# Kernel optimization log

Hardware: AMD Instinct MI355X
Metric: run time of the kernel (lower is better)

The kernel has to match this reference:

```python
import jax, jax.numpy as jnp
import numpy as np
from jax import lax

B, D, T = 16, 256, 8192
N_CB, CB_SIZE, CB_DIM = 7, 1024, 8
EPS = 1e-12


def setup_inputs() -> dict:
    key = jax.random.key(0)
    ks = jax.random.split(key, 9)
    z = jax.random.normal(ks[0], (B, D, T), dtype=jnp.float32)
    # weight-normalized 1x1 conv params (v direction, g magnitude, bias)
    in_v = jax.random.normal(ks[1], (N_CB, CB_DIM, D), dtype=jnp.float32) * 0.05
    in_g = jax.random.uniform(ks[2], (N_CB, CB_DIM), minval=0.5, maxval=1.5, dtype=jnp.float32)
    in_b = jax.random.normal(ks[3], (N_CB, CB_DIM), dtype=jnp.float32) * 0.01
    out_v = jax.random.normal(ks[4], (N_CB, D, CB_DIM), dtype=jnp.float32) * 0.05
    out_g = jax.random.uniform(ks[5], (N_CB, D), minval=0.5, maxval=1.5, dtype=jnp.float32)
    out_b = jax.random.normal(ks[6], (N_CB, D), dtype=jnp.float32) * 0.01
    codebooks = jax.random.normal(ks[7], (N_CB, CB_SIZE, CB_DIM), dtype=jnp.float32)
    return {"z": z, "in_v": in_v, "in_g": in_g, "in_b": in_b,
            "out_v": out_v, "out_g": out_g, "out_b": out_b,
            "codebooks": codebooks, "n_quantizers": 7}


def _wn(v, g):
    # torch weight_norm dim=0: per-output-channel direction * magnitude
    return g[:, None] * v / jnp.linalg.norm(v, axis=1, keepdims=True)


def _l2norm(x):
    return x / jnp.maximum(jnp.linalg.norm(x, axis=-1, keepdims=True), EPS)


def reference(z, in_v, in_g, in_b, out_v, out_g, out_b, codebooks, n_quantizers):
    b = z.shape[0]
    residual = z
    z_q = jnp.zeros_like(z)
    commitment_loss = jnp.float32(0.0)
    codebook_loss = jnp.float32(0.0)
    all_indices = []
    for i in range(N_CB):
        w_in = _wn(in_v[i], in_g[i])            # [cd, D]
        z_e = jnp.einsum('cd,bdt->bct', w_in, residual) + in_b[i][None, :, None]  # [B, cd, T]
        enc = z_e.transpose(0, 2, 1).reshape(-1, CB_DIM)        # [(B T), cd]
        enc_n = _l2norm(enc)
        cb_n = _l2norm(codebooks[i])                             # [K, cd]
        dist = (jnp.sum(enc_n**2, axis=1, keepdims=True)
                - 2.0 * enc_n @ cb_n.T
                + jnp.sum(cb_n**2, axis=1)[None, :])             # [(B T), K]
        idx = jnp.argmin(dist, axis=1).reshape(b, -1)            # [B, T]
        z_q_c = codebooks[i][idx].transpose(0, 2, 1)             # [B, cd, T]
        commit_i = jnp.mean((z_e - lax.stop_gradient(z_q_c))**2, axis=(1, 2))  # [B]
        cbl_i = jnp.mean((z_q_c - lax.stop_gradient(z_e))**2, axis=(1, 2))     # [B]
        z_q_ste = z_e + lax.stop_gradient(z_q_c - z_e)
        w_out = _wn(out_v[i], out_g[i])          # [D, cd]
        z_q_i = jnp.einsum('dc,bct->bdt', w_out, z_q_ste) + out_b[i][None, :, None]
        mask = (jnp.full((b,), i) < n_quantizers).astype(z.dtype)  # [B]
        z_q = z_q + z_q_i * mask[:, None, None]
        residual = residual - z_q_i
        commitment_loss = commitment_loss + jnp.mean(commit_i * mask)
        codebook_loss = codebook_loss + jnp.mean(cbl_i * mask)
        all_indices.append(idx)
    return z_q, commitment_loss, codebook_loss, jnp.stack(all_indices, axis=1)
```

## Files before the change

kernel.cpp:

```cpp
#include <hip/hip_runtime.h>
#include <math.h>

#define NCB 7
#define CBK 1024
#define CD  8
#define BB  16
#define DD  256
#define TT  8192

static constexpr size_t ZQN  = (size_t)BB * DD * TT;
static constexpr size_t IDX0 = ZQN + 2;

__global__ void rvq_prep(const float* __restrict__ in_v, const float* __restrict__ in_g,
                         const float* __restrict__ out_v, const float* __restrict__ out_g,
                         const float* __restrict__ cb,
                         float* __restrict__ wTin, float* __restrict__ wTout,
                         float* __restrict__ cbp, double* __restrict__ lossAcc)
{
#pragma clang fp contract(off)
  int gid = blockIdx.x * blockDim.x + threadIdx.x;
  if (gid == 0) *lossAcc = 0.0;
  if (gid < NCB*DD*CD) {
    int i = gid / (DD*CD); int rem = gid % (DD*CD); int d = rem / CD; int c = rem % CD;
    const float* vrow = in_v + ((size_t)i*CD + c) * DD;
    double acc = 0.0;
    for (int q = 0; q < DD; ++q) { double v = vrow[q]; acc += v*v; }
    float nf = (float)sqrt(acc);
    wTin[((size_t)i*DD + d)*CD + c] = (in_g[i*CD + c] * vrow[d]) / nf;
  } else if (gid < 2*NCB*DD*CD) {
    int e = gid - NCB*DD*CD;
    int i = e / (DD*CD); int rem = e % (DD*CD); int d = rem / CD; int c = rem % CD;
    const float* vrow = out_v + ((size_t)i*DD + d)*CD;
    double acc = 0.0;
    for (int q = 0; q < CD; ++q) { double v = vrow[q]; acc += v*v; }
    float nf = (float)sqrt(acc);
    wTout[((size_t)i*DD + d)*CD + c] = (out_g[i*DD + d] * vrow[c]) / nf;
  } else if (gid < 2*NCB*DD*CD + NCB*CBK) {
    int e = gid - 2*NCB*DD*CD;
    int i = e / CBK; int k = e % CBK;
    const float* row = cb + ((size_t)i*CBK + k)*CD;
    double acc = 0.0;
    for (int c = 0; c < CD; ++c) { double v = row[c]; acc += v*v; }
    float nf = fmaxf((float)sqrt(acc), 1e-12f);
    float* orow = cbp + ((size_t)i*CBK + k)*16;
    float c2 = 0.f;
    for (int c = 0; c < CD; ++c) {
      float cn = row[c] / nf;
      orow[c] = cn;
      float q = cn*cn; c2 += q;
    }
    orow[8] = c2;
  }
}

__launch_bounds__(256, 2)
__global__ void rvq_main(const float* __restrict__ z,
                         const float* __restrict__ in_b, const float* __restrict__ out_b,
                         const float* __restrict__ cb,
                         const int* __restrict__ nqp,
                         const float* __restrict__ wTin, const float* __restrict__ wTout,
                         const float* __restrict__ cbp,
                         float* __restrict__ out, double* __restrict__ lossAcc)
{
#pragma clang fp contract(off)
  const int tid = threadIdx.x;
  const int p   = tid & 63;
  const int wu  = __builtin_amdgcn_readfirstlane(tid >> 6);
  const int blk = blockIdx.x;
  const int b   = blk >> 7;
  const int t0  = (blk & 127) << 6;
  int nq = *nqp; nq = nq < 0 ? 0 : (nq > NCB ? NCB : nq);

  __shared__ float zep[4][64][CD];
  __shared__ float encn[64][CD];
  __shared__ float zef[64][CD];
  __shared__ float aval[64];
  __shared__ float bdist[4][64];
  __shared__ int   bkix[4][64];
  __shared__ float zst[64][CD];

  const float* zbase = z + ((size_t)b*DD + wu*64)*TT + t0 + p;
  float* zqbase = out + ((size_t)b*DD + wu*64)*TT + t0 + p;

  float r[64];
#pragma unroll
  for (int j = 0; j < 64; ++j) r[j] = zbase[(size_t)j*TT];

  if (nq == 0) {
#pragma unroll 8
    for (int j = 0; j < 64; ++j) zqbase[(size_t)j*TT] = 0.f;
  }

  double lacc = 0.0;

  for (int i = 0; i < NCB; ++i) {
    float ze[CD];
#pragma unroll
    for (int c = 0; c < CD; ++c) ze[c] = 0.f;
    const float* wrow = wTin + ((size_t)i*DD + wu*64)*CD;
#pragma unroll 8
    for (int j = 0; j < 64; ++j) {
      float rv = r[j];
#pragma unroll
      for (int c = 0; c < CD; ++c) ze[c] = fmaf(wrow[j*CD + c], rv, ze[c]);
    }
#pragma unroll
    for (int c = 0; c < CD; ++c) zep[wu][p][c] = ze[c];
    __syncthreads();

    if (tid < 64) {
      float zfull[CD];
#pragma unroll
      for (int c = 0; c < CD; ++c) {
        float s = ((zep[0][p][c] + zep[1][p][c]) + zep[2][p][c]) + zep[3][p][c];
        zfull[c] = s + in_b[i*CD + c];
      }
      float ss = 0.f;
#pragma unroll
      for (int c = 0; c < CD; ++c) { float q = zfull[c]*zfull[c]; ss += q; }
      float den = fmaxf(sqrtf(ss), 1e-12f);
      float a2 = 0.f;
#pragma unroll
      for (int c = 0; c < CD; ++c) {
        float en = zfull[c] / den;
        encn[p][c] = en;
        zef[p][c]  = zfull[c];
        float q = en*en; a2 += q;
      }
      aval[p] = a2;
    }
    __syncthreads();

    float en[CD];
#pragma unroll
    for (int c = 0; c < CD; ++c) en[c] = encn[p][c];
    float a2 = aval[p];
    const float* crow = cbp + ((size_t)i*CBK + wu*256)*16;
    float best = 3.0e38f; int bk = 0;
#pragma unroll 4
    for (int kk = 0; kk < 256; ++kk) {
      const float* rw = crow + kk*16;
      float m = en[0]*rw[0];
#pragma unroll
      for (int c = 1; c < CD; ++c) m = fmaf(en[c], rw[c], m);
      float dd = fmaf(-2.f, m, a2) + rw[8];
      bool lt = dd < best;
      best = lt ? dd : best;
      bk   = lt ? kk : bk;
    }
    bdist[wu][p] = best; bkix[wu][p] = wu*256 + bk;
    __syncthreads();

    if (tid < 64) {
      float bb_ = bdist[0][p]; int k = bkix[0][p];
#pragma unroll
      for (int ww = 1; ww < 4; ++ww) {
        float dv = bdist[ww][p]; int kv = bkix[ww][p];
        bool lt = dv < bb_;
        bb_ = lt ? dv : bb_;
        k   = lt ? kv : k;
      }
      const float* qrow = cb + ((size_t)i*CBK + k)*CD;
      float sloc = 0.f;
#pragma unroll
      for (int c = 0; c < CD; ++c) {
        float zc = qrow[c];
        float zv = zef[p][c];
        zst[p][c] = zv + (zc - zv);
        float df = zv - zc;
        float q = df*df; sloc += q;
      }
      if (i < nq) lacc += (double)sloc;
      out[IDX0 + ((size_t)b*NCB + i)*TT + t0 + p] = (float)k;
    }
    __syncthreads();

    float zs[CD];
#pragma unroll
    for (int c = 0; c < CD; ++c) zs[c] = zst[p][c];
    const float* worow = wTout + ((size_t)i*DD + wu*64)*CD;
    const float* obrow = out_b + i*DD + wu*64;
#pragma unroll 8
    for (int j = 0; j < 64; ++j) {
      float m = worow[j*CD]*zs[0];
#pragma unroll
      for (int c = 1; c < CD; ++c) m = fmaf(worow[j*CD + c], zs[c], m);
      float zqi = m + obrow[j];
      r[j] -= zqi;
    }
    if (i == nq - 1) {
#pragma unroll 8
      for (int j = 0; j < 64; ++j)
        zqbase[(size_t)j*TT] = zbase[(size_t)j*TT] - r[j];
    }
    __syncthreads();
  }

  if (tid < 64) {
#pragma unroll
    for (int off = 32; off >= 1; off >>= 1) lacc += __shfl_down(lacc, off, 64);
    if (p == 0) atomicAdd(lossAcc, lacc);
  }
}

__global__ void rvq_fin(const double* __restrict__ lossAcc, float* __restrict__ out) {
  float v = (float)(*lossAcc * (1.0 / 1048576.0));
  out[ZQN]     = v;
  out[ZQN + 1] = v;
}

extern "C" void kernel_launch(void* const* d_in, const int* in_sizes, int n_in,
                              void* d_out, int out_size, void* d_ws, size_t ws_size,
                              hipStream_t stream) {
  const float* z     = (const float*)d_in[0];
  const float* in_v  = (const float*)d_in[1];
  const float* in_g  = (const float*)d_in[2];
  const float* in_b  = (const float*)d_in[3];
  const float* out_v = (const float*)d_in[4];
  const float* out_g = (const float*)d_in[5];
  const float* out_b = (const float*)d_in[6];
  const float* cb    = (const float*)d_in[7];
  const int*   nqp   = (const int*)d_in[8];
  float* out = (float*)d_out;

  double* lossAcc = (double*)d_ws;
  float* wTin  = (float*)((char*)d_ws + 64);
  float* wTout = wTin  + (size_t)NCB*DD*CD;
  float* cbp   = wTout + (size_t)NCB*DD*CD;

  rvq_prep<<<140, 256, 0, stream>>>(in_v, in_g, out_v, out_g, cb,
                                    wTin, wTout, cbp, lossAcc);
  rvq_main<<<BB * (TT/64), 256, 0, stream>>>(z, in_b, out_b, cb, nqp,
                                             wTin, wTout, cbp, out, lossAcc);
  rvq_fin<<<1, 1, 0, stream>>>(lossAcc, out);
}
```

Baseline: 880.2 us.

## Use packed FP32 FMAs, redundant per-wave reductions, and fewer barriers in RVQ kernel

Packs the codebook as interleaved pairs of entries so the nearest-neighbour search evaluates two codewords per packed v2f FMA, and vectorises the input projection the same way. Every wave now redundantly finishes the cross-wave reduction, normalisation and argmin merge in registers instead of having wave 0 do it and broadcast through shared memory. This removes two barriers per codebook and the serial single-wave phases. It also raises launch bounds to 4 blocks per CU, which risks register pressure given the 64-float residual array and full unrolls.

```diff
diff --git a/kernel.cpp b/kernel.cpp
--- a/kernel.cpp
+++ b/kernel.cpp
@@ -7,6 +7,9 @@
 #define BB  16
 #define DD  256
 #define TT  8192
+
+typedef float v2f __attribute__((ext_vector_type(2)));
+typedef float v4f __attribute__((ext_vector_type(4)));
 
 static constexpr size_t ZQN  = (size_t)BB * DD * TT;
 static constexpr size_t IDX0 = ZQN + 2;
@@ -42,18 +45,19 @@
     double acc = 0.0;
     for (int c = 0; c < CD; ++c) { double v = row[c]; acc += v*v; }
     float nf = fmaxf((float)sqrt(acc), 1e-12f);
-    float* orow = cbp + ((size_t)i*CBK + k)*16;
+    float* rec = cbp + ((size_t)i*512 + (k >> 1))*32;
+    int h = k & 1;
     float c2 = 0.f;
     for (int c = 0; c < CD; ++c) {
       float cn = row[c] / nf;
-      orow[c] = cn;
-      float q = cn*cn; c2 += q;
-    }
-    orow[8] = c2;
-  }
-}
-
-__launch_bounds__(256, 2)
+      rec[2*c + h] = cn;
+      float s = cn*cn; c2 += s;
+    }
+    rec[16 + h] = c2;
+  }
+}
+
+__launch_bounds__(256, 4)
 __global__ void rvq_main(const float* __restrict__ z,
                          const float* __restrict__ in_b, const float* __restrict__ out_b,
                          const float* __restrict__ cb,
@@ -71,13 +75,9 @@
   const int t0  = (blk & 127) << 6;
   int nq = *nqp; nq = nq < 0 ? 0 : (nq > NCB ? NCB : nq);
 
-  __shared__ float zep[4][64][CD];
-  __shared__ float encn[64][CD];
-  __shared__ float zef[64][CD];
-  __shared__ float aval[64];
+  __shared__ float zep[4][CD][64];
   __shared__ float bdist[4][64];
   __shared__ int   bkix[4][64];
-  __shared__ float zst[64][CD];
 
   const float* zbase = z + ((size_t)b*DD + wu*64)*TT + t0 + p;
   float* zqbase = out + ((size_t)b*DD + wu*64)*TT + t0 + p;
@@ -87,113 +87,112 @@
   for (int j = 0; j < 64; ++j) r[j] = zbase[(size_t)j*TT];
 
   if (nq == 0) {
-#pragma unroll 8
+#pragma unroll
     for (int j = 0; j < 64; ++j) zqbase[(size_t)j*TT] = 0.f;
   }
 
   double lacc = 0.0;
 
   for (int i = 0; i < NCB; ++i) {
-    float ze[CD];
-#pragma unroll
-    for (int c = 0; c < CD; ++c) ze[c] = 0.f;
-    const float* wrow = wTin + ((size_t)i*DD + wu*64)*CD;
-#pragma unroll 8
+    v2f ze2[4];
+#pragma unroll
+    for (int h = 0; h < 4; ++h) ze2[h] = (v2f){0.f, 0.f};
+    const v2f* wrow2 = (const v2f*)(wTin + ((size_t)i*DD + wu*64)*CD);
+#pragma unroll
     for (int j = 0; j < 64; ++j) {
-      float rv = r[j];
-#pragma unroll
-      for (int c = 0; c < CD; ++c) ze[c] = fmaf(wrow[j*CD + c], rv, ze[c]);
-    }
-#pragma unroll
-    for (int c = 0; c < CD; ++c) zep[wu][p][c] = ze[c];
+      v2f rv2 = (v2f){r[j], r[j]};
+#pragma unroll
+      for (int h = 0; h < 4; ++h)
+        ze2[h] = __builtin_elementwise_fma(wrow2[j*4 + h], rv2, ze2[h]);
+    }
+#pragma unroll
+    for (int h = 0; h < 4; ++h) {
+      zep[wu][2*h    ][p] = ze2[h].x;
+      zep[wu][2*h + 1][p] = ze2[h].y;
+    }
     __syncthreads();
 
-    if (tid < 64) {
-      float zfull[CD];
-#pragma unroll
-      for (int c = 0; c < CD; ++c) {
-        float s = ((zep[0][p][c] + zep[1][p][c]) + zep[2][p][c]) + zep[3][p][c];
-        zfull[c] = s + in_b[i*CD + c];
-      }
-      float ss = 0.f;
-#pragma unroll
-      for (int c = 0; c < CD; ++c) { float q = zfull[c]*zfull[c]; ss += q; }
-      float den = fmaxf(sqrtf(ss), 1e-12f);
-      float a2 = 0.f;
-#pragma unroll
-      for (int c = 0; c < CD; ++c) {
-        float en = zfull[c] / den;
-        encn[p][c] = en;
-        zef[p][c]  = zfull[c];
-        float q = en*en; a2 += q;
-      }
-      aval[p] = a2;
-    }
+    float zef[CD], en[CD];
+    float ss = 0.f;
+#pragma unroll
+    for (int c = 0; c < CD; ++c) {
+      float s  = ((zep[0][c][p] + zep[1][c][p]) + zep[2][c][p]) + zep[3][c][p];
+      float zf = s + in_b[i*CD + c];
+      zef[c] = zf;
+      float sq = zf*zf; ss += sq;
+    }
+    float den = fmaxf(sqrtf(ss), 1e-12f);
+    float a2 = 0.f;
+#pragma unroll
+    for (int c = 0; c < CD; ++c) {
+      float e = zef[c] / den;
+      en[c] = e;
+      float sq = e*e; a2 += sq;
+    }
+
+    v2f enb[CD];
+#pragma unroll
+    for (int c = 0; c < CD; ++c) enb[c] = (v2f){en[c], en[c]};
+    const v2f a2b = (v2f){a2, a2};
+    const v2f n2b = (v2f){-2.f, -2.f};
+    const v2f* crow = (const v2f*)(cbp + ((size_t)i*512 + wu*128)*32);
+    float best = 3.0e38f; int bk = 0;
+#pragma unroll 2
+    for (int qq = 0; qq < 128; ++qq) {
+      const v2f* rw = crow + qq*16;
+      v2f m = enb[0]*rw[0];
+#pragma unroll
+      for (int c = 1; c < CD; ++c) m = __builtin_elementwise_fma(enb[c], rw[c], m);
+      v2f dd = __builtin_elementwise_fma(n2b, m, a2b);
+      dd = dd + rw[8];
+      int k0 = (wu*128 + qq)*2;
+      bool l0 = dd.x < best; best = l0 ? dd.x : best; bk = l0 ? k0     : bk;
+      bool l1 = dd.y < best; best = l1 ? dd.y : best; bk = l1 ? k0 + 1 : bk;
+    }
+    bdist[wu][p] = best; bkix[wu][p] = bk;
     __syncthreads();
 
-    float en[CD];
-#pragma unroll
-    for (int c = 0; c < CD; ++c) en[c] = encn[p][c];
-    float a2 = aval[p];
-    const float* crow = cbp + ((size_t)i*CBK + wu*256)*16;
-    float best = 3.0e38f; int bk = 0;
-#pragma unroll 4
-    for (int kk = 0; kk < 256; ++kk) {
-      const float* rw = crow + kk*16;
-      float m = en[0]*rw[0];
-#pragma unroll
-      for (int c = 1; c < CD; ++c) m = fmaf(en[c], rw[c], m);
-      float dd = fmaf(-2.f, m, a2) + rw[8];
-      bool lt = dd < best;
-      best = lt ? dd : best;
-      bk   = lt ? kk : bk;
-    }
-    bdist[wu][p] = best; bkix[wu][p] = wu*256 + bk;
-    __syncthreads();
-
-    if (tid < 64) {
-      float bb_ = bdist[0][p]; int k = bkix[0][p];
-#pragma unroll
-      for (int ww = 1; ww < 4; ++ww) {
-        float dv = bdist[ww][p]; int kv = bkix[ww][p];
-        bool lt = dv < bb_;
-        bb_ = lt ? dv : bb_;
-        k   = lt ? kv : k;
-      }
-      const float* qrow = cb + ((size_t)i*CBK + k)*CD;
-      float sloc = 0.f;
-#pragma unroll
-      for (int c = 0; c < CD; ++c) {
-        float zc = qrow[c];
-        float zv = zef[p][c];
-        zst[p][c] = zv + (zc - zv);
-        float df = zv - zc;
-        float q = df*df; sloc += q;
-      }
+    float bb_ = bdist[0][p]; int k = bkix[0][p];
+#pragma unroll
+    for (int ww = 1; ww < 4; ++ww) {
+      float dv = bdist[ww][p]; int kv = bkix[ww][p];
+      bool lt = dv < bb_;
+      bb_ = lt ? dv : bb_;
+      k   = lt ? kv : k;
+    }
+    const float* qrow = cb + ((size_t)i*CBK + k)*CD;
+    v4f qa = ((const v4f*)qrow)[0];
+    v4f qb = ((const v4f*)qrow)[1];
+    float zc[CD] = {qa.x, qa.y, qa.z, qa.w, qb.x, qb.y, qb.z, qb.w};
+    float zst[CD];
+    float sloc = 0.f;
+#pragma unroll
+    for (int c = 0; c < CD; ++c) {
+      float zv = zef[c];
+      zst[c] = zv + (zc[c] - zv);
+      float df = zv - zc[c];
+      float sq = df*df; sloc += sq;
+    }
+    if (wu == 0) {
       if (i < nq) lacc += (double)sloc;
       out[IDX0 + ((size_t)b*NCB + i)*TT + t0 + p] = (float)k;
     }
-    __syncthreads();
-
-    float zs[CD];
-#pragma unroll
-    for (int c = 0; c < CD; ++c) zs[c] = zst[p][c];
+
     const float* worow = wTout + ((size_t)i*DD + wu*64)*CD;
     const float* obrow = out_b + i*DD + wu*64;
-#pragma unroll 8
+#pragma unroll
     for (int j = 0; j < 64; ++j) {
-      float m = worow[j*CD]*zs[0];
-#pragma unroll
-      for (int c = 1; c < CD; ++c) m = fmaf(worow[j*CD + c], zs[c], m);
+      float m = worow[j*CD]*zst[0];
+#pragma unroll
+      for (int c = 1; c < CD; ++c) m = fmaf(worow[j*CD + c], zst[c], m);
       float zqi = m + obrow[j];
       r[j] -= zqi;
     }
     if (i == nq - 1) {
-#pragma unroll 8
+#pragma unroll
       for (int j = 0; j < 64; ++j)
         zqbase[(size_t)j*TT] = zbase[(size_t)j*TT] - r[j];
     }
-    __syncthreads();
   }
 
   if (tid < 64) {
```

Measured after the change: 1.577 ms. 79.2% more time.
